# Optimization experiments

Measured on AMD Instinct MI355X. Metric: run time of the kernel, lower is better.

The kernel has to match this reference:

```python
import jax, jax.numpy as jnp
import numpy as np

def setup_inputs() -> dict:
    key = jax.random.key(0)
    k1, k2 = jax.random.split(key)
    bb_feats = jax.random.normal(k1, (8, 512, 128, 128), dtype=jnp.float32)
    aux_out = jax.random.normal(k2, (8, 19, 128, 128), dtype=jnp.float32)
    return {"bb_feats": bb_feats, "aux_out": aux_out}

def reference(bb_feats, aux_out):
    B, K, H, W = aux_out.shape
    C = bb_feats.shape[1]
    probs = jax.nn.softmax(aux_out.reshape(B, K, H * W), axis=2)  # [B,K,HW]
    feats = bb_feats.reshape(B, C, H * W)                          # [B,C,HW]
    # weighted sum over spatial dim: [B,K,HW] x [B,C,HW] -> [B,K,C]
    ctx = jnp.einsum('bks,bcs->bkc', probs, feats)
    # -> [B,C,K,1]
    return jnp.transpose(ctx, (0, 2, 1))[..., None]
```

## Files before the change

### kernel.cpp

```cpp
#include <hip/hip_runtime.h>
#include <math.h>

#define B 8
#define C 512
#define K 19
#define HW 16384
#define ROWS (B * K)
#define L2E 1.44269504088896340736f

#define NW 4
#define CPW 4
#define CPB (CPW * NW)
#define CG (C / CPB)
#define NSC 4
#define SCHUNK (HW / NSC)
#define TS 256
#define NT (SCHUNK / TS)

typedef __attribute__((address_space(3))) unsigned int lds_u32;
typedef const __attribute__((address_space(1))) unsigned int glb_u32;

__global__ __launch_bounds__(1024)
void probs_kernel(const float* __restrict__ aux, float* __restrict__ probs) {
    int row  = blockIdx.x;
    int tid  = threadIdx.x;
    int lane = tid & 63;
    int wave = tid >> 6;
    __shared__ float red[16];

    const float4* x4 = (const float4*)(aux + (size_t)row * HW);
    float4*       p4 = (float4*)(probs + (size_t)row * HW);

    float4 v[4];
    #pragma unroll
    for (int i = 0; i < 4; i++) v[i] = x4[tid + i * 1024];

    float m = -INFINITY;
    #pragma unroll
    for (int i = 0; i < 4; i++)
        m = fmaxf(m, fmaxf(fmaxf(v[i].x, v[i].y), fmaxf(v[i].z, v[i].w)));
    #pragma unroll
    for (int off = 32; off > 0; off >>= 1) m = fmaxf(m, __shfl_xor(m, off, 64));
    if (lane == 0) red[wave] = m;
    __syncthreads();
    #pragma unroll
    for (int w = 0; w < 16; w++) m = fmaxf(m, red[w]);
    __syncthreads();

    float nm = -m * L2E;
    float s = 0.f;
    #pragma unroll
    for (int i = 0; i < 4; i++) {
        v[i].x = exp2f(fmaf(v[i].x, L2E, nm));
        v[i].y = exp2f(fmaf(v[i].y, L2E, nm));
        v[i].z = exp2f(fmaf(v[i].z, L2E, nm));
        v[i].w = exp2f(fmaf(v[i].w, L2E, nm));
        s += (v[i].x + v[i].y) + (v[i].z + v[i].w);
    }
    #pragma unroll
    for (int off = 32; off > 0; off >>= 1) s += __shfl_xor(s, off, 64);
    if (lane == 0) red[wave] = s;
    __syncthreads();
    float Z = 0.f;
    #pragma unroll
    for (int w = 0; w < 16; w++) Z += red[w];
    float inv = 1.0f / Z;

    #pragma unroll
    for (int i = 0; i < 4; i++) {
        float4 o;
        o.x = v[i].x * inv; o.y = v[i].y * inv;
        o.z = v[i].z * inv; o.w = v[i].w * inv;
        p4[tid + i * 1024] = o;
    }
}

__global__ __launch_bounds__(256)
__attribute__((amdgpu_waves_per_eu(2)))
void gather_kernel(const float* __restrict__ feats, const float* __restrict__ probs,
                   float* __restrict__ out) {
    __shared__ float plds[2][K][TS];

    int bid = blockIdx.x;
    int xcd = bid & 7;
    int lid = xcd * 128 + (bid >> 3);
    int cg  = lid & (CG - 1);
    int grp = lid >> 5;
    int sc  = grp & (NSC - 1);
    int b   = grp >> 2;

    int tid  = threadIdx.x;
    int lane = tid & 63;
    int wave = tid >> 6;
    int c0   = cg * CPB + wave * CPW;

    const float* Pbase = probs + (size_t)b * K * HW + sc * SCHUNK;
    const float* Fbase = feats + ((size_t)b * C + c0) * HW + sc * SCHUNK;

    float acc[CPW][K];
    #pragma unroll
    for (int c = 0; c < CPW; c++)
        #pragma unroll
        for (int k = 0; k < K; k++) acc[c][k] = 0.f;

    for (int k = wave; k < K; k += NW)
        __builtin_amdgcn_global_load_lds((glb_u32*)(Pbase + (size_t)k * HW + lane * 4),
                                         (lds_u32*)&plds[0][k][0], 16, 0, 0);
    float4 f_cur[CPW], f_next[CPW];
    #pragma unroll
    for (int c = 0; c < CPW; c++)
        f_cur[c] = *(const float4*)(Fbase + c * HW + lane * 4);

    for (int t = 0; t < NT; t++) {
        int buf = t & 1;
        __syncthreads();

        if (t + 1 < NT) {
            int s1 = (t + 1) * TS;
            #pragma unroll
            for (int c = 0; c < CPW; c++)
                f_next[c] = *(const float4*)(Fbase + c * HW + s1 + lane * 4);
            for (int k = wave; k < K; k += NW)
                __builtin_amdgcn_global_load_lds((glb_u32*)(Pbase + (size_t)k * HW + s1 + lane * 4),
                                                 (lds_u32*)&plds[buf ^ 1][k][0], 16, 0, 0);
        }

        #pragma unroll
        for (int k = 0; k < K; k++) {
            float4 pv = *(const float4*)(&plds[buf][k][lane * 4]);
            #pragma unroll
            for (int c = 0; c < CPW; c++) {
                acc[c][k] = fmaf(pv.x, f_cur[c].x, acc[c][k]);
                acc[c][k] = fmaf(pv.y, f_cur[c].y, acc[c][k]);
                acc[c][k] = fmaf(pv.z, f_cur[c].z, acc[c][k]);
                acc[c][k] = fmaf(pv.w, f_cur[c].w, acc[c][k]);
            }
        }
        #pragma unroll
        for (int c = 0; c < CPW; c++) f_cur[c] = f_next[c];
    }

    #pragma unroll
    for (int c = 0; c < CPW; c++)
        #pragma unroll
        for (int k = 0; k < K; k++) {
            float v = acc[c][k];
            #pragma unroll
            for (int off = 32; off > 0; off >>= 1) v += __shfl_xor(v, off, 64);
            if (lane == 0)
                atomicAdd(&out[((size_t)b * C + c0 + c) * K + k], v);
        }
}

extern "C" void kernel_launch(void* const* d_in, const int* in_sizes, int n_in,
                              void* d_out, int out_size, void* d_ws, size_t ws_size,
                              hipStream_t stream) {
    const float* feats = (const float*)d_in[0];
    const float* aux   = (const float*)d_in[1];
    float* out   = (float*)d_out;
    float* probs = (float*)d_ws;

    hipMemsetAsync(d_out, 0, (size_t)out_size * sizeof(float), stream);
    probs_kernel<<<ROWS, 1024, 0, stream>>>(aux, probs);
    gather_kernel<<<B * CG * NSC, 256, 0, stream>>>(feats, probs, out);
}
```

Baseline: 395.0 us.

## Read probabilities directly from global memory and fold output zeroing into softmax kernel

The gather kernel no longer stages probability tiles in LDS with async global-to-LDS loads and block barriers. Each wave now loads its probability float4s straight from global (L2/cache), software-pipelined one k ahead. The separate memset of the output is replaced by having the first 19 softmax blocks zero the output buffer, which removes one launch. In exchange, every wave re-reads the same probability data from cache instead of sharing it through LDS, which raises cache traffic and exposes more load latency.

Result: slower. 434.7 us (+10.0%).

```diff
diff --git a/kernel.cpp b/kernel.cpp
--- a/kernel.cpp
+++ b/kernel.cpp
@@ -17,16 +17,17 @@
 #define TS 256
 #define NT (SCHUNK / TS)
 
-typedef __attribute__((address_space(3))) unsigned int lds_u32;
-typedef const __attribute__((address_space(1))) unsigned int glb_u32;
-
 __global__ __launch_bounds__(1024)
-void probs_kernel(const float* __restrict__ aux, float* __restrict__ probs) {
+void probs_kernel(const float* __restrict__ aux, float* __restrict__ probs,
+                  float* __restrict__ out) {
     int row  = blockIdx.x;
     int tid  = threadIdx.x;
     int lane = tid & 63;
     int wave = tid >> 6;
     __shared__ float red[16];
+
+    if (row < 19)
+        ((float4*)out)[(size_t)row * 1024 + tid] = make_float4(0.f, 0.f, 0.f, 0.f);
 
     const float4* x4 = (const float4*)(aux + (size_t)row * HW);
     float4*       p4 = (float4*)(probs + (size_t)row * HW);
@@ -79,8 +80,6 @@
 __attribute__((amdgpu_waves_per_eu(2)))
 void gather_kernel(const float* __restrict__ feats, const float* __restrict__ probs,
                    float* __restrict__ out) {
-    __shared__ float plds[2][K][TS];
-
     int bid = blockIdx.x;
     int xcd = bid & 7;
     int lid = xcd * 128 + (bid >> 3);
@@ -94,7 +93,7 @@
     int wave = tid >> 6;
     int c0   = cg * CPB + wave * CPW;
 
-    const float* Pbase = probs + (size_t)b * K * HW + sc * SCHUNK;
+    const float* Pbase = probs + (size_t)b * K * HW + sc * SCHUNK + lane * 4;
     const float* Fbase = feats + ((size_t)b * C + c0) * HW + sc * SCHUNK;
 
     float acc[CPW][K];
@@ -103,39 +102,36 @@
         #pragma unroll
         for (int k = 0; k < K; k++) acc[c][k] = 0.f;
 
-    for (int k = wave; k < K; k += NW)
-        __builtin_amdgcn_global_load_lds((glb_u32*)(Pbase + (size_t)k * HW + lane * 4),
-                                         (lds_u32*)&plds[0][k][0], 16, 0, 0);
     float4 f_cur[CPW], f_next[CPW];
     #pragma unroll
     for (int c = 0; c < CPW; c++)
         f_cur[c] = *(const float4*)(Fbase + c * HW + lane * 4);
 
     for (int t = 0; t < NT; t++) {
-        int buf = t & 1;
-        __syncthreads();
-
+        int s = t * TS;
         if (t + 1 < NT) {
-            int s1 = (t + 1) * TS;
+            int s1 = s + TS;
             #pragma unroll
             for (int c = 0; c < CPW; c++)
                 f_next[c] = *(const float4*)(Fbase + c * HW + s1 + lane * 4);
-            for (int k = wave; k < K; k += NW)
-                __builtin_amdgcn_global_load_lds((glb_u32*)(Pbase + (size_t)k * HW + s1 + lane * 4),
-                                                 (lds_u32*)&plds[buf ^ 1][k][0], 16, 0, 0);
         }
 
+        float4 p_cur = *(const float4*)(Pbase + s);
         #pragma unroll
         for (int k = 0; k < K; k++) {
-            float4 pv = *(const float4*)(&plds[buf][k][lane * 4]);
+            float4 p_nxt;
+            if (k + 1 < K)
+                p_nxt = *(const float4*)(Pbase + (size_t)(k + 1) * HW + s);
             #pragma unroll
             for (int c = 0; c < CPW; c++) {
-                acc[c][k] = fmaf(pv.x, f_cur[c].x, acc[c][k]);
-                acc[c][k] = fmaf(pv.y, f_cur[c].y, acc[c][k]);
-                acc[c][k] = fmaf(pv.z, f_cur[c].z, acc[c][k]);
-                acc[c][k] = fmaf(pv.w, f_cur[c].w, acc[c][k]);
+                acc[c][k] = fmaf(p_cur.x, f_cur[c].x, acc[c][k]);
+                acc[c][k] = fmaf(p_cur.y, f_cur[c].y, acc[c][k]);
+                acc[c][k] = fmaf(p_cur.z, f_cur[c].z, acc[c][k]);
+                acc[c][k] = fmaf(p_cur.w, f_cur[c].w, acc[c][k]);
             }
+            p_cur = p_nxt;
         }
+
         #pragma unroll
         for (int c = 0; c < CPW; c++) f_cur[c] = f_next[c];
     }
@@ -160,7 +156,6 @@
     float* out   = (float*)d_out;
     float* probs = (float*)d_ws;
 
-    hipMemsetAsync(d_out, 0, (size_t)out_size * sizeof(float), stream);
-    probs_kernel<<<ROWS, 1024, 0, stream>>>(aux, probs);
+    probs_kernel<<<ROWS, 1024, 0, stream>>>(aux, probs, out);
     gather_kernel<<<B * CG * NSC, 256, 0, stream>>>(feats, probs, out);
 }
```
